# Optimization experiments

Hardware: AMD Instinct MI355X
Metric: run time of the kernel (lower is better)

## Reference

```python
import jax, jax.numpy as jnp
import numpy as np

B, S, E, H = 4, 2048, 1024, 16
D = E // H  # head_size = 64

def setup_inputs() -> dict:
    key = jax.random.key(0)
    ks = jax.random.split(key, 10)
    s_e = E ** -0.5
    s_4e = (4 * E) ** -0.5
    inp = {
        "x": jax.random.normal(ks[0], (B, S, E), dtype=jnp.float32),
        # per-head Q/K/V weights, stacked: [H, E, D], no bias
        "Wq": jax.random.normal(ks[1], (H, E, D), dtype=jnp.float32) * s_e,
        "Wk": jax.random.normal(ks[2], (H, E, D), dtype=jnp.float32) * s_e,
        "Wv": jax.random.normal(ks[3], (H, E, D), dtype=jnp.float32) * s_e,
        "Wo": jax.random.normal(ks[4], (E, E), dtype=jnp.float32) * s_e,
        "bo": jax.random.normal(ks[5], (E,), dtype=jnp.float32) * 0.01,
        "W1": jax.random.normal(ks[6], (E, 4 * E), dtype=jnp.float32) * s_e,
        "b1": jax.random.normal(ks[7], (4 * E,), dtype=jnp.float32) * 0.01,
        "W2": jax.random.normal(ks[8], (4 * E, E), dtype=jnp.float32) * s_4e,
        "b2": jax.random.normal(ks[9], (E,), dtype=jnp.float32) * 0.01,
    }
    return inp

def reference(x, Wq, Wk, Wv, Wo, bo, W1, b1, W2, b2):
    b, s, e = x.shape
    # NOTE: original scales by embedding_size**-0.5 (Size of x), not head_size
    scale = e ** -0.5
    q = jnp.einsum("bse,hed->bhsd", x, Wq)
    k = jnp.einsum("bse,hed->bhsd", x, Wk)
    v = jnp.einsum("bse,hed->bhsd", x, Wv)
    scores = jnp.einsum("bhsd,bhtd->bhst", q, k) * scale
    causal = jnp.tril(jnp.ones((s, s), dtype=bool))
    scores = jnp.where(causal, scores, -jnp.inf)
    weights = jax.nn.softmax(scores, axis=-1)
    attn = jnp.einsum("bhst,bhtd->bhsd", weights, v)  # [B,H,S,D]
    # concat heads along last dim: [B,S,H*D]
    attn = attn.transpose(0, 2, 1, 3).reshape(b, s, e)
    y = attn @ Wo + bo
    x = x + y  # residual (no LayerNorm applied in original forward)
    h = jax.nn.relu(x @ W1 + b1)
    ffn = h @ W2 + b2
    return x + ffn
```

## Files before the change

### kernel.cpp

```cpp
#include <hip/hip_runtime.h>
#include <stdint.h>

#define B_ 4
#define S_ 2048
#define E_ 1024
#define H_ 16
#define D_ 64

typedef unsigned short u16;
typedef u16 u16x8 __attribute__((ext_vector_type(8)));
typedef __bf16 bf16x8 __attribute__((ext_vector_type(8)));
typedef float f32x4 __attribute__((ext_vector_type(4)));

__device__ __forceinline__ float bf2f(u16 x) {
  unsigned int v = ((unsigned int)x) << 16;
  return __builtin_bit_cast(float, v);
}
__device__ __forceinline__ u16 f2bf(float f) {
  unsigned int u = __builtin_bit_cast(unsigned int, f);
  unsigned int r = (u + 0x7fffu + ((u >> 16) & 1u)) >> 16;
  return (u16)r;
}

__device__ __forceinline__ void gl2lds16(const u16* g, u16* l) {
  __builtin_amdgcn_global_load_lds(
      (const __attribute__((address_space(1))) void*)g,
      (__attribute__((address_space(3))) void*)l, 16, 0, 0);
}

__global__ __launch_bounds__(256) void cast_bf16_k(const float* __restrict__ src,
                                                   u16* __restrict__ dst, long n) {
  long i = ((long)blockIdx.x * 256 + threadIdx.x) * 8;
  if (i + 8 <= n) {
    f32x4 a = *(const f32x4*)(src + i), b = *(const f32x4*)(src + i + 4);
    u16x8 o;
#pragma unroll
    for (int j = 0; j < 4; j++) { o[j] = f2bf(a[j]); o[j + 4] = f2bf(b[j]); }
    *(u16x8*)(dst + i) = o;
  }
}

__global__ __launch_bounds__(256) void castT_k(const float* __restrict__ src,
                                               u16* __restrict__ dst, int R, int C) {
  long bofs = (long)blockIdx.z * R * C;
  src += bofs; dst += bofs;
  __shared__ u16 t[32][33];
  int c0 = blockIdx.x * 32, r0 = blockIdx.y * 32;
  int lc = threadIdx.x & 31, lr8 = threadIdx.x >> 5;
#pragma unroll
  for (int i = 0; i < 4; i++) {
    int lr = lr8 + i * 8;
    t[lr][lc] = f2bf(src[(long)(r0 + lr) * C + c0 + lc]);
  }
  __syncthreads();
#pragma unroll
  for (int i = 0; i < 4; i++) {
    int lr = lr8 + i * 8;
    dst[(long)(c0 + lr) * R + r0 + lc] = t[lc][lr];
  }
}

__global__ __launch_bounds__(256) void vT_k(const u16* __restrict__ QKV,
                                            u16* __restrict__ VTg) {
  int bh = blockIdx.z, d0 = blockIdx.y * 32, t0 = blockIdx.x * 32;
  int b = bh >> 4, h = bh & 15;
  __shared__ u16 t[32][33];
  int lc = threadIdx.x & 31, lr8 = threadIdx.x >> 5;
#pragma unroll
  for (int i = 0; i < 4; i++) {
    int lr = lr8 + i * 8;
    t[lr][lc] = QKV[(long)(b * S_ + t0 + lr) * 3072 + 2048 + h * 64 + d0 + lc];
  }
  __syncthreads();
#pragma unroll
  for (int i = 0; i < 4; i++) {
    int lr = lr8 + i * 8;
    VTg[((long)bh * 64 + d0 + lr) * S_ + t0 + lc] = t[lc][lr];
  }
}

template <bool AF32, bool CF32>
__global__ __launch_bounds__(256) void gemm128(const void* __restrict__ Av,
                                               const u16* __restrict__ BT,
                                               void* __restrict__ Cv,
                                               const float* __restrict__ bias,
                                               const float* __restrict__ resid,
                                               int M, int N, int K, int relu,
                                               u16* __restrict__ Cbf) {
  __shared__ u16 As[128 * 32];
  __shared__ u16 Bs[128 * 32];
  const int tid = threadIdx.x;
  const int wave = tid >> 6, lane = tid & 63;
  const int m0 = blockIdx.y * 128, n0 = blockIdx.x * 128;
  const int wm = wave >> 1, wn = wave & 1;
  const int fr = lane & 15, quad = lane >> 4;

  f32x4 acc[4][4] = {};

  const int srow = wave * 32 + (lane >> 2);
  const int skcol = (lane & 3) * 8;

  for (int k0 = 0; k0 < K; k0 += 32) {
    __syncthreads();
    if (AF32) {
      const float* Ap = (const float*)Av + (long)(m0 + (tid >> 1)) * K + k0 + (tid & 1) * 16;
      f32x4 f0 = *(const f32x4*)Ap, f1 = *(const f32x4*)(Ap + 4);
      f32x4 f2 = *(const f32x4*)(Ap + 8), f3 = *(const f32x4*)(Ap + 12);
      u16x8 p0, p1;
#pragma unroll
      for (int j = 0; j < 4; j++) {
        p0[j] = f2bf(f0[j]); p0[j + 4] = f2bf(f1[j]);
        p1[j] = f2bf(f2[j]); p1[j + 4] = f2bf(f3[j]);
      }
      *(u16x8*)&As[(tid >> 1) * 32 + (tid & 1) * 16] = p0;
      *(u16x8*)&As[(tid >> 1) * 32 + (tid & 1) * 16 + 8] = p1;
    } else {
      const u16* Ag = (const u16*)Av + (long)(m0 + srow) * K + k0 + skcol;
      gl2lds16(Ag, &As[(wave * 32) * 32]);
      gl2lds16(Ag + 16 * (long)K, &As[(wave * 32 + 16) * 32]);
    }
    {
      const u16* Bg = BT + (long)(n0 + srow) * K + k0 + skcol;
      gl2lds16(Bg, &Bs[(wave * 32) * 32]);
      gl2lds16(Bg + 16 * (long)K, &Bs[(wave * 32 + 16) * 32]);
    }
    __syncthreads();

    bf16x8 af[4], bfr[4];
#pragma unroll
    for (int mi = 0; mi < 4; mi++)
      af[mi] = __builtin_bit_cast(bf16x8, *(const u16x8*)&As[(wm * 64 + mi * 16 + fr) * 32 + quad * 8]);
#pragma unroll
    for (int ni = 0; ni < 4; ni++)
      bfr[ni] = __builtin_bit_cast(bf16x8, *(const u16x8*)&Bs[(wn * 64 + ni * 16 + fr) * 32 + quad * 8]);
#pragma unroll
    for (int mi = 0; mi < 4; mi++)
#pragma unroll
      for (int ni = 0; ni < 4; ni++)
        acc[mi][ni] = __builtin_amdgcn_mfma_f32_16x16x32_bf16(af[mi], bfr[ni], acc[mi][ni], 0, 0, 0);
  }

#pragma unroll
  for (int mi = 0; mi < 4; mi++)
#pragma unroll
    for (int ni = 0; ni < 4; ni++)
#pragma unroll
      for (int r = 0; r < 4; r++) {
        int gm = m0 + wm * 64 + mi * 16 + quad * 4 + r;
        int gn = n0 + wn * 64 + ni * 16 + fr;
        float v = acc[mi][ni][r];
        if (bias) v += bias[gn];
        if (resid) v += resid[(long)gm * N + gn];
        if (relu) v = fmaxf(v, 0.f);
        if (CF32) ((float*)Cv)[(long)gm * N + gn] = v;
        else      ((u16*)Cv)[(long)gm * N + gn] = f2bf(v);
        if (Cbf) Cbf[(long)gm * N + gn] = f2bf(v);
      }
}

__global__ __launch_bounds__(256) void attn_mfma3(const u16* __restrict__ QKV,
                                                  const u16* __restrict__ VTg,
                                                  u16* __restrict__ attn) {
  int p = blockIdx.x, h = blockIdx.y, b = blockIdx.z;
  int tid = threadIdx.x;
  int wq = tid >> 6, lane = tid & 63;
  int fr = lane & 15, quad = lane >> 4;
  int kf = quad * 8;

  __shared__ u16 Qs[64][72];
  __shared__ u16 Ks[64][72];
  __shared__ u16 Vt[64][72];
  __shared__ u16 Ps[4][16][72];

  const u16* base = QKV + (long)b * S_ * 3072;
  const u16* vbase = VTg + (long)(b * 16 + h) * 64 * S_;
  int st = tid >> 2;
  int sd = (tid & 3) * 16;

  for (int ti = 0; ti < 2; ti++) {
    int qt = ti ? (31 - p) : p;

    {
      const u16* qr = base + (long)(qt * 64 + st) * 3072 + h * 64 + sd;
      u16x8 a = *(const u16x8*)qr, d = *(const u16x8*)(qr + 8);
      u16x8 oa, od;
#pragma unroll
      for (int j = 0; j < 8; j++) {
        oa[j] = f2bf(bf2f(a[j]) * 0.03125f);
        od[j] = f2bf(bf2f(d[j]) * 0.03125f);
      }
      *(u16x8*)&Qs[st][sd] = oa;
      *(u16x8*)&Qs[st][sd + 8] = od;
    }
    __syncthreads();
    bf16x8 qf0 = __builtin_bit_cast(bf16x8, *(const u16x8*)&Qs[wq * 16 + fr][kf]);
    bf16x8 qf1 = __builtin_bit_cast(bf16x8, *(const u16x8*)&Qs[wq * 16 + fr][32 + kf]);

    f32x4 acc[4] = {};
    float m[4], l[4];
#pragma unroll
    for (int r = 0; r < 4; r++) { m[r] = -INFINITY; l[r] = 0.f; }

    for (int c = 0; c <= qt; c++) {
      int t0 = c * 64;
      __syncthreads();
      {
        const u16* kr = base + (long)(t0 + st) * 3072 + 1024 + h * 64 + sd;
        u16x8 k0 = *(const u16x8*)kr, k1 = *(const u16x8*)(kr + 8);
        const u16* vr = vbase + (long)st * S_ + t0 + sd;
        u16x8 v0 = *(const u16x8*)vr, v1 = *(const u16x8*)(vr + 8);
        *(u16x8*)&Ks[st][sd] = k0;
        *(u16x8*)&Ks[st][sd + 8] = k1;
        *(u16x8*)&Vt[st][sd] = v0;
        *(u16x8*)&Vt[st][sd + 8] = v1;
      }
      __syncthreads();

      f32x4 sc[4] = {};
#pragma unroll
      for (int nt = 0; nt < 4; nt++) {
        bf16x8 b0 = __builtin_bit_cast(bf16x8, *(const u16x8*)&Ks[nt * 16 + fr][kf]);
        bf16x8 b1 = __builtin_bit_cast(bf16x8, *(const u16x8*)&Ks[nt * 16 + fr][32 + kf]);
        sc[nt] = __builtin_amdgcn_mfma_f32_16x16x32_bf16(qf0, b0, sc[nt], 0, 0, 0);
        sc[nt] = __builtin_amdgcn_mfma_f32_16x16x32_bf16(qf1, b1, sc[nt], 0, 0, 0);
      }

      if (c == qt) {
        int qloc = wq * 16 + quad * 4;
#pragma unroll
        for (int nt = 0; nt < 4; nt++)
#pragma unroll
          for (int r = 0; r < 4; r++)
            if (nt * 16 + fr > qloc + r) sc[nt][r] = -1e30f;
      }

      float al[4], ps[4];
#pragma unroll
      for (int r = 0; r < 4; r++) {
        float v = fmaxf(fmaxf(sc[0][r], sc[1][r]), fmaxf(sc[2][r], sc[3][r]));
#pragma unroll
        for (int off = 1; off < 16; off <<= 1) v = fmaxf(v, __shfl_xor(v, off));
        float mn = fmaxf(m[r], v);
        al[r] = __expf(m[r] - mn);
        m[r] = mn;
        ps[r] = 0.f;
      }
#pragma unroll
      for (int nt = 0; nt < 4; nt++)
#pragma unroll
        for (int r = 0; r < 4; r++) {
          float pv = __expf(sc[nt][r] - m[r]);
          sc[nt][r] = pv;
          ps[r] += pv;
        }
#pragma unroll
      for (int r = 0; r < 4; r++) {
#pragma unroll
        for (int off = 1; off < 16; off <<= 1) ps[r] += __shfl_xor(ps[r], off);
        l[r] = l[r] * al[r] + ps[r];
#pragma unroll
        for (int nt = 0; nt < 4; nt++) acc[nt][r] *= al[r];
      }

#pragma unroll
      for (int nt = 0; nt < 4; nt++)
#pragma unroll
        for (int r = 0; r < 4; r++)
          Ps[wq][quad * 4 + r][nt * 16 + fr] = f2bf(sc[nt][r]);

      bf16x8 pa0 = __builtin_bit_cast(bf16x8, *(const u16x8*)&Ps[wq][fr][kf]);
      bf16x8 pa1 = __builtin_bit_cast(bf16x8, *(const u16x8*)&Ps[wq][fr][32 + kf]);
#pragma unroll
      for (int nt = 0; nt < 4; nt++) {
        bf16x8 vb0 = __builtin_bit_cast(bf16x8, *(const u16x8*)&Vt[nt * 16 + fr][kf]);
        bf16x8 vb1 = __builtin_bit_cast(bf16x8, *(const u16x8*)&Vt[nt * 16 + fr][32 + kf]);
        acc[nt] = __builtin_amdgcn_mfma_f32_16x16x32_bf16(pa0, vb0, acc[nt], 0, 0, 0);
        acc[nt] = __builtin_amdgcn_mfma_f32_16x16x32_bf16(pa1, vb1, acc[nt], 0, 0, 0);
      }
    }

    long row = (long)b * S_ + qt * 64 + wq * 16 + quad * 4;
#pragma unroll
    for (int nt = 0; nt < 4; nt++)
#pragma unroll
      for (int r = 0; r < 4; r++)
        attn[(row + r) * 1024 + h * 64 + nt * 16 + fr] = f2bf(acc[nt][r] / l[r]);
  }
}

extern "C" void kernel_launch(void* const* d_in, const int* in_sizes, int n_in,
                              void* d_out, int out_size, void* d_ws, size_t ws_size,
                              hipStream_t stream) {
  (void)in_sizes; (void)n_in; (void)out_size;
  const float* x  = (const float*)d_in[0];
  const float* Wq = (const float*)d_in[1];
  const float* Wk = (const float*)d_in[2];
  const float* Wv = (const float*)d_in[3];
  const float* Wo = (const float*)d_in[4];
  const float* bo = (const float*)d_in[5];
  const float* W1 = (const float*)d_in[6];
  const float* b1 = (const float*)d_in[7];
  const float* W2 = (const float*)d_in[8];
  const float* b2 = (const float*)d_in[9];
  float* out = (float*)d_out;

  char* ws = (char*)d_ws;
  u16*   QKV  = (u16*)(ws);
  u16*   attn = (u16*)(ws + 50331648);
  u16*   hbuf = (u16*)(ws);
  float* x1   = (float*)(ws + 67108864);
  u16*   VTg  = (u16*)(ws + 67108864);
  u16*   xb   = (u16*)(ws + 83886080);
  u16*   WT   = (u16*)(ws + 100663296);
  u16*   WoT  = (u16*)(ws + 106954752);
  u16*   W1T  = (u16*)(ws + 109051904);
  u16*   W2T  = (u16*)(ws + 117440512);
  u16*   x1b  = (u16*)(ws + 125829120);
  bool bigws = ws_size >= (size_t)142606336;

  cast_bf16_k<<<4096, 256, 0, stream>>>(x, xb, (long)8192 * 1024);
  castT_k<<<dim3(2, 32, 16), 256, 0, stream>>>(Wq, WT, 1024, 64);
  castT_k<<<dim3(2, 32, 16), 256, 0, stream>>>(Wk, WT + 1048576, 1024, 64);
  castT_k<<<dim3(2, 32, 16), 256, 0, stream>>>(Wv, WT + 2097152, 1024, 64);
  castT_k<<<dim3(32, 32, 1), 256, 0, stream>>>(Wo, WoT, 1024, 1024);
  castT_k<<<dim3(128, 32, 1), 256, 0, stream>>>(W1, W1T, 1024, 4096);
  castT_k<<<dim3(32, 128, 1), 256, 0, stream>>>(W2, W2T, 4096, 1024);

  gemm128<false, false><<<dim3(24, 64), 256, 0, stream>>>(xb, WT, QKV, nullptr, nullptr, 8192, 3072, 1024, 0, nullptr);
  vT_k<<<dim3(64, 2, 64), 256, 0, stream>>>(QKV, VTg);
  attn_mfma3<<<dim3(16, H_, B_), 256, 0, stream>>>(QKV, VTg, attn);
  gemm128<false, true><<<dim3(8, 64), 256, 0, stream>>>(attn, WoT, x1, bo, x, 8192, 1024, 1024, 0, bigws ? x1b : nullptr);
  if (bigws)
    gemm128<false, false><<<dim3(32, 64), 256, 0, stream>>>(x1b, W1T, hbuf, b1, nullptr, 8192, 4096, 1024, 1, nullptr);
  else
    gemm128<true, false><<<dim3(32, 64), 256, 0, stream>>>(x1, W1T, hbuf, b1, nullptr, 8192, 4096, 1024, 1, nullptr);
  gemm128<false, true><<<dim3(8, 64), 256, 0, stream>>>(hbuf, W2T, out, b2, x1, 8192, 1024, 4096, 0, nullptr);
}
```

Baseline: 667.5 us.

## Add 256x256 tiled bf16 MFMA GEMM with XCD swizzle and staged double buffering

Introduces a 512-thread GEMM kernel with 256x256 output tiles, 128 KB of LDS double-buffered in 64-wide K steps, a swizzled LDS layout, and global-to-LDS staging interleaved with four MFMA phases per K step using setprio and explicit waitcnt. Workgroup IDs are remapped so consecutive tiles land on the same XCD. It replaces the 128x128 GEMM for the QKV, output-projection, FFN1 and FFN2 launches. The aim is more operand reuse per LDS load and overlap of memory traffic with compute. The cost is heavy register pressure and fewer workgroups per GEMM (128 for the N=1024 GEMMs), which may underfill the GPU.

```diff
diff --git a/kernel.cpp b/kernel.cpp
--- a/kernel.cpp
+++ b/kernel.cpp
@@ -158,6 +158,177 @@
       }
 }
 
+__device__ __forceinline__ bf16x8 ldfrag(const u16* base, int r, int kk, int quad) {
+  int u = (((r << 5) + (quad << 3) + (kk << 13)) ^ (((r >> 3) & 1) << 4));
+  return __builtin_bit_cast(bf16x8, *(const u16x8*)(base + u));
+}
+
+__device__ __forceinline__ void stage_half_g(const u16* __restrict__ G, int ldk,
+                                             int row0, int k0,
+                                             u16* __restrict__ region,
+                                             int half, int tid) {
+  int r = half * 128 + (tid >> 2);
+  int c = ((tid & 3) << 3) ^ (((r >> 3) & 1) << 4);
+  const u16* g = G + (size_t)(row0 + r) * ldk + k0 + c;
+  u16* l = region + half * 4096 + (tid >> 6) * 512;
+  gl2lds16(g, l);
+  gl2lds16(g + 32, l + 8192);
+}
+
+template <bool CF32>
+__global__ __launch_bounds__(512) void gemm256(const u16* __restrict__ A,
+                                               const u16* __restrict__ BT,
+                                               void* __restrict__ Cv,
+                                               const float* __restrict__ bias,
+                                               const float* __restrict__ resid,
+                                               int M, int N, int K, int relu,
+                                               u16* __restrict__ Cbf) {
+  (void)M;
+  __shared__ u16 sm[65536];
+  const int tid = threadIdx.x;
+  const int wave = tid >> 6, lane = tid & 63;
+  const int wm = wave >> 2, wn = wave & 3;
+  const int fr = lane & 15, quad = lane >> 4;
+
+  const int nbx = gridDim.x;
+  const int nwg = nbx * (int)gridDim.y;
+  const int wgid = blockIdx.y * nbx + blockIdx.x;
+  const int qq = nwg >> 3, rr = nwg & 7;
+  const int xcd = wgid & 7, loc = wgid >> 3;
+  const int sw = (xcd < rr ? xcd * (qq + 1) : rr * (qq + 1) + (xcd - rr) * qq) + loc;
+  const int n0 = (sw % nbx) * 256;
+  const int m0 = (sw / nbx) * 256;
+
+  const int NT = K >> 6;
+
+  f32x4 acc[8][4] = {};
+
+  u16* buf0 = sm;
+  u16* buf1 = sm + 32768;
+
+  stage_half_g(A, K, m0, 0, buf0, 0, tid);
+  stage_half_g(A, K, m0, 0, buf0, 1, tid);
+  stage_half_g(BT, K, n0, 0, buf0 + 16384, 0, tid);
+  stage_half_g(BT, K, n0, 0, buf0 + 16384, 1, tid);
+  if (NT > 1) {
+    stage_half_g(A, K, m0, 64, buf1, 0, tid);
+    stage_half_g(A, K, m0, 64, buf1, 1, tid);
+    asm volatile("s_waitcnt vmcnt(4)" ::: "memory");
+  } else {
+    asm volatile("s_waitcnt vmcnt(0)" ::: "memory");
+  }
+  __builtin_amdgcn_s_barrier();
+
+  for (int t = 0; t < NT; ++t) {
+    u16* cb = (t & 1) ? buf1 : buf0;
+    u16* nb = (t & 1) ? buf0 : buf1;
+    const int kn = (t + 1) << 6;
+    const int k2 = (t + 2) << 6;
+    const bool st1 = (t + 1) < NT;
+    const bool st2 = (t + 2) < NT;
+
+    bf16x8 a0[4][2], a1[4][2], b0[2][2], b1[2][2];
+
+#pragma unroll
+    for (int mi = 0; mi < 4; ++mi)
+#pragma unroll
+      for (int kk = 0; kk < 2; ++kk)
+        a0[mi][kk] = ldfrag(cb, wm * 128 + mi * 16 + fr, kk, quad);
+#pragma unroll
+    for (int ni = 0; ni < 2; ++ni)
+#pragma unroll
+      for (int kk = 0; kk < 2; ++kk)
+        b0[ni][kk] = ldfrag(cb + 16384, wn * 64 + ni * 16 + fr, kk, quad);
+    if (st1) stage_half_g(BT, K, n0, kn, nb + 16384, 0, tid);
+    __builtin_amdgcn_s_barrier();
+    asm volatile("s_waitcnt lgkmcnt(0)" ::: "memory");
+    __builtin_amdgcn_sched_barrier(0);
+    __builtin_amdgcn_s_setprio(1);
+#pragma unroll
+    for (int mi = 0; mi < 4; ++mi)
+#pragma unroll
+      for (int ni = 0; ni < 2; ++ni)
+#pragma unroll
+        for (int kk = 0; kk < 2; ++kk)
+          acc[mi][ni] = __builtin_amdgcn_mfma_f32_16x16x32_bf16(a0[mi][kk], b0[ni][kk], acc[mi][ni], 0, 0, 0);
+    __builtin_amdgcn_s_setprio(0);
+    __builtin_amdgcn_s_barrier();
+
+#pragma unroll
+    for (int mi = 0; mi < 4; ++mi)
+#pragma unroll
+      for (int kk = 0; kk < 2; ++kk)
+        a1[mi][kk] = ldfrag(cb, wm * 128 + (mi + 4) * 16 + fr, kk, quad);
+    if (st1) stage_half_g(BT, K, n0, kn, nb + 16384, 1, tid);
+    __builtin_amdgcn_s_barrier();
+    asm volatile("s_waitcnt lgkmcnt(0)" ::: "memory");
+    __builtin_amdgcn_sched_barrier(0);
+    __builtin_amdgcn_s_setprio(1);
+#pragma unroll
+    for (int mi = 0; mi < 4; ++mi)
+#pragma unroll
+      for (int ni = 0; ni < 2; ++ni)
+#pragma unroll
+        for (int kk = 0; kk < 2; ++kk)
+          acc[mi + 4][ni] = __builtin_amdgcn_mfma_f32_16x16x32_bf16(a1[mi][kk], b0[ni][kk], acc[mi + 4][ni], 0, 0, 0);
+    __builtin_amdgcn_s_setprio(0);
+    __builtin_amdgcn_s_barrier();
+
+#pragma unroll
+    for (int ni = 0; ni < 2; ++ni)
+#pragma unroll
+      for (int kk = 0; kk < 2; ++kk)
+        b1[ni][kk] = ldfrag(cb + 16384, wn * 64 + (ni + 2) * 16 + fr, kk, quad);
+    if (st2) stage_half_g(A, K, m0, k2, cb, 0, tid);
+    __builtin_amdgcn_s_barrier();
+    asm volatile("s_waitcnt lgkmcnt(0)" ::: "memory");
+    __builtin_amdgcn_sched_barrier(0);
+    __builtin_amdgcn_s_setprio(1);
+#pragma unroll
+    for (int mi = 0; mi < 4; ++mi)
+#pragma unroll
+      for (int ni = 0; ni < 2; ++ni)
+#pragma unroll
+        for (int kk = 0; kk < 2; ++kk)
+          acc[mi + 4][ni + 2] = __builtin_amdgcn_mfma_f32_16x16x32_bf16(a1[mi][kk], b1[ni][kk], acc[mi + 4][ni + 2], 0, 0, 0);
+    __builtin_amdgcn_s_setprio(0);
+    __builtin_amdgcn_s_barrier();
+
+    if (st2) stage_half_g(A, K, m0, k2, cb, 1, tid);
+    if (st2) asm volatile("s_waitcnt vmcnt(4)" ::: "memory");
+    else     asm volatile("s_waitcnt vmcnt(0)" ::: "memory");
+    __builtin_amdgcn_s_barrier();
+    __builtin_amdgcn_sched_barrier(0);
+    __builtin_amdgcn_s_setprio(1);
+#pragma unroll
+    for (int mi = 0; mi < 4; ++mi)
+#pragma unroll
+      for (int ni = 0; ni < 2; ++ni)
+#pragma unroll
+        for (int kk = 0; kk < 2; ++kk)
+          acc[mi][ni + 2] = __builtin_amdgcn_mfma_f32_16x16x32_bf16(a0[mi][kk], b1[ni][kk], acc[mi][ni + 2], 0, 0, 0);
+    __builtin_amdgcn_s_setprio(0);
+    __builtin_amdgcn_s_barrier();
+  }
+
+#pragma unroll
+  for (int mi = 0; mi < 8; ++mi)
+#pragma unroll
+    for (int ni = 0; ni < 4; ++ni)
+#pragma unroll
+      for (int r = 0; r < 4; ++r) {
+        int gm = m0 + wm * 128 + mi * 16 + quad * 4 + r;
+        int gn = n0 + wn * 64 + ni * 16 + fr;
+        float v = acc[mi][ni][r];
+        if (bias) v += bias[gn];
+        if (resid) v += resid[(long)gm * N + gn];
+        if (relu) v = fmaxf(v, 0.f);
+        if (CF32) ((float*)Cv)[(long)gm * N + gn] = v;
+        else      ((u16*)Cv)[(long)gm * N + gn] = f2bf(v);
+        if (Cbf) Cbf[(long)gm * N + gn] = f2bf(v);
+      }
+}
+
 __global__ __launch_bounds__(256) void attn_mfma3(const u16* __restrict__ QKV,
                                                   const u16* __restrict__ VTg,
                                                   u16* __restrict__ attn) {
@@ -326,13 +497,13 @@
   castT_k<<<dim3(128, 32, 1), 256, 0, stream>>>(W1, W1T, 1024, 4096);
   castT_k<<<dim3(32, 128, 1), 256, 0, stream>>>(W2, W2T, 4096, 1024);
 
-  gemm128<false, false><<<dim3(24, 64), 256, 0, stream>>>(xb, WT, QKV, nullptr, nullptr, 8192, 3072, 1024, 0, nullptr);
+  gemm256<false><<<dim3(12, 32), 512, 0, stream>>>(xb, WT, QKV, nullptr, nullptr, 8192, 3072, 1024, 0, nullptr);
   vT_k<<<dim3(64, 2, 64), 256, 0, stream>>>(QKV, VTg);
   attn_mfma3<<<dim3(16, H_, B_), 256, 0, stream>>>(QKV, VTg, attn);
-  gemm128<false, true><<<dim3(8, 64), 256, 0, stream>>>(attn, WoT, x1, bo, x, 8192, 1024, 1024, 0, bigws ? x1b : nullptr);
+  gemm256<true><<<dim3(4, 32), 512, 0, stream>>>(attn, WoT, x1, bo, x, 8192, 1024, 1024, 0, bigws ? x1b : nullptr);
   if (bigws)
-    gemm128<false, false><<<dim3(32, 64), 256, 0, stream>>>(x1b, W1T, hbuf, b1, nullptr, 8192, 4096, 1024, 1, nullptr);
+    gemm256<false><<<dim3(16, 32), 512, 0, stream>>>(x1b, W1T, hbuf, b1, nullptr, 8192, 4096, 1024, 1, nullptr);
   else
     gemm128<true, false><<<dim3(32, 64), 256, 0, stream>>>(x1, W1T, hbuf, b1, nullptr, 8192, 4096, 1024, 1, nullptr);
-  gemm128<false, true><<<dim3(8, 64), 256, 0, stream>>>(hbuf, W2T, out, b2, x1, 8192, 1024, 4096, 0, nullptr);
-}
+  gemm256<true><<<dim3(4, 32), 512, 0, stream>>>(hbuf, W2T, out, b2, x1, 8192, 1024, 4096, 0, nullptr);
+}
```

After: 702.1 us. 5.2% more time.

## Replace 128-tile GEMMs with 256-row 512-thread pipelined GEMM kernel

Applied to the files above, without the earlier changes.

Adds a new gemm256 kernel with 256xBN tiles, 8 waves, and double-buffered direct global-to-LDS staging using XOR swizzle. It interleaves MFMA quadrants with next-tile loads, raises wave priority around MFMAs, and remaps workgroups for XCD locality. The QKV, output projection, FFN1 and FFN2 GEMMs switch to it. The larger tiles raise data reuse, but they use more LDS and registers and leave fewer workgroups for the smaller GEMMs.

```diff
diff --git a/kernel.cpp b/kernel.cpp
--- a/kernel.cpp
+++ b/kernel.cpp
@@ -158,6 +158,163 @@
       }
 }
 
+__device__ __forceinline__ bf16x8 ldfragS(const u16* base, int r, int kk, int quad, int SL) {
+  int u = (((r << 5) + (quad << 3) + kk * SL)) ^ (((r >> 3) & 1) << 4);
+  return __builtin_bit_cast(bf16x8, *(const u16x8*)(base + u));
+}
+
+__device__ __forceinline__ void stage_half(const u16* __restrict__ G, int ldk,
+                                           int row0, int k0,
+                                           u16* __restrict__ region,
+                                           int half, int tid, int SLu) {
+  int r = half * 128 + (tid >> 2);
+  int c = ((tid & 3) << 3) ^ (((r >> 3) & 1) << 4);
+  const u16* g = G + (size_t)(row0 + r) * ldk + k0 + c;
+  u16* l = region + half * 4096 + (tid >> 6) * 512;
+  gl2lds16(g, l);
+  gl2lds16(g + 32, l + SLu);
+}
+
+#define MFMA_Q(ML, NL)                                                         \
+  __builtin_amdgcn_s_setprio(1);                                               \
+  _Pragma("unroll") for (int mi = 0; mi < MH; ++mi)                            \
+  _Pragma("unroll") for (int ni = 0; ni < NH; ++ni)                            \
+  _Pragma("unroll") for (int kk = 0; kk < 2; ++kk)                             \
+      acc[(ML) + mi][(NL) + ni] = __builtin_amdgcn_mfma_f32_16x16x32_bf16(     \
+          aF[(ML) + mi][kk], bF[(NL) + ni][kk], acc[(ML) + mi][(NL) + ni],     \
+          0, 0, 0);                                                            \
+  __builtin_amdgcn_s_setprio(0);
+
+template <int BN, bool CF32>
+__global__ __launch_bounds__(512) void gemm256(const u16* __restrict__ A,
+                                               const u16* __restrict__ BT,
+                                               void* __restrict__ Cv,
+                                               const float* __restrict__ bias,
+                                               const float* __restrict__ resid,
+                                               int M, int N, int K, int relu,
+                                               u16* __restrict__ Cbf) {
+  (void)M;
+  constexpr int WM = (BN == 256) ? 2 : 4;
+  constexpr int WN = 8 / WM;
+  constexpr int MI = 256 / (WM * 16);
+  constexpr int NI = BN / (WN * 16);
+  constexpr int MH = MI / 2, NH = NI / 2;
+  constexpr int BSL = BN * 32;
+  constexpr int BUFU = 16384 + BN * 64;
+  constexpr int BH = BN / 128;
+  constexpr int NREADS = (MI + NI) * 2;
+
+  __shared__ u16 sm[2 * BUFU];
+  const int tid = threadIdx.x;
+  const int wave = tid >> 6, lane = tid & 63;
+  const int wm = wave / WN, wn = wave % WN;
+  const int fr = lane & 15, quad = lane >> 4;
+
+  const int nbx = gridDim.x;
+  const int nwg = nbx * (int)gridDim.y;
+  const int wgid = blockIdx.y * nbx + blockIdx.x;
+  const int qq = nwg >> 3, rr = nwg & 7;
+  const int xcd = wgid & 7, loc = wgid >> 3;
+  const int sw = (xcd < rr ? xcd * (qq + 1) : rr * (qq + 1) + (xcd - rr) * qq) + loc;
+  const int n0 = (sw % nbx) * BN;
+  const int m0 = (sw / nbx) * 256;
+
+  const int NT = K >> 6;
+
+  f32x4 acc[MI][NI] = {};
+
+  u16* buf0 = sm;
+  u16* buf1 = sm + BUFU;
+
+  const int rAbase = wm * (256 / WM) + fr;
+  const int rBbase = wn * 64 + fr;
+
+  stage_half(A, K, m0, 0, buf0, 0, tid, 8192);
+  stage_half(A, K, m0, 0, buf0, 1, tid, 8192);
+  stage_half(BT, K, n0, 0, buf0 + 16384, 0, tid, BSL);
+  if (BH == 2) stage_half(BT, K, n0, 0, buf0 + 16384, 1, tid, BSL);
+  if (NT > 1) {
+    stage_half(A, K, m0, 64, buf1, 0, tid, 8192);
+    stage_half(A, K, m0, 64, buf1, 1, tid, 8192);
+    stage_half(BT, K, n0, 64, buf1 + 16384, 0, tid, BSL);
+    if (BH == 2) stage_half(BT, K, n0, 64, buf1 + 16384, 1, tid, BSL);
+    if constexpr (BN == 256) asm volatile("s_waitcnt vmcnt(8)" ::: "memory");
+    else                     asm volatile("s_waitcnt vmcnt(6)" ::: "memory");
+  } else {
+    asm volatile("s_waitcnt vmcnt(0)" ::: "memory");
+  }
+  __builtin_amdgcn_s_barrier();
+
+  for (int t = 0; t < NT; ++t) {
+    u16* cb = (t & 1) ? buf1 : buf0;
+    const int k2 = (t + 2) << 6;
+    const bool st2 = (t + 2) < NT;
+
+    bf16x8 aF[MI][2], bF[NI][2];
+
+#pragma unroll
+    for (int mi = 0; mi < MH; ++mi)
+#pragma unroll
+      for (int kk = 0; kk < 2; ++kk)
+        aF[mi][kk] = ldfragS(cb, rAbase + mi * 16, kk, quad, 8192);
+#pragma unroll
+    for (int ni = 0; ni < NH; ++ni)
+#pragma unroll
+      for (int kk = 0; kk < 2; ++kk)
+        bF[ni][kk] = ldfragS(cb + 16384, rBbase + ni * 16, kk, quad, BSL);
+#pragma unroll
+    for (int mi = MH; mi < MI; ++mi)
+#pragma unroll
+      for (int kk = 0; kk < 2; ++kk)
+        aF[mi][kk] = ldfragS(cb, rAbase + mi * 16, kk, quad, 8192);
+#pragma unroll
+    for (int ni = NH; ni < NI; ++ni)
+#pragma unroll
+      for (int kk = 0; kk < 2; ++kk)
+        bF[ni][kk] = ldfragS(cb + 16384, rBbase + ni * 16, kk, quad, BSL);
+    __builtin_amdgcn_sched_group_barrier(0x100 , NREADS, 0);
+
+    MFMA_Q(0, 0)
+    MFMA_Q(MH, 0)
+    __builtin_amdgcn_s_barrier();
+    if (st2) {
+      stage_half(A, K, m0, k2, cb, 0, tid, 8192);
+      stage_half(A, K, m0, k2, cb, 1, tid, 8192);
+    }
+    MFMA_Q(MH, NH)
+    __builtin_amdgcn_s_barrier();
+    if (st2) {
+      stage_half(BT, K, n0, k2, cb + 16384, 0, tid, BSL);
+      if (BH == 2) stage_half(BT, K, n0, k2, cb + 16384, 1, tid, BSL);
+    }
+    MFMA_Q(0, NH)
+    if (st2) {
+      if constexpr (BN == 256) asm volatile("s_waitcnt vmcnt(8)" ::: "memory");
+      else                     asm volatile("s_waitcnt vmcnt(6)" ::: "memory");
+    } else {
+      asm volatile("s_waitcnt vmcnt(0)" ::: "memory");
+    }
+    __builtin_amdgcn_s_barrier();
+  }
+
+#pragma unroll
+  for (int mi = 0; mi < MI; ++mi)
+#pragma unroll
+    for (int ni = 0; ni < NI; ++ni)
+#pragma unroll
+      for (int r = 0; r < 4; ++r) {
+        int gm = m0 + wm * (256 / WM) + mi * 16 + quad * 4 + r;
+        int gn = n0 + wn * 64 + ni * 16 + fr;
+        float v = acc[mi][ni][r];
+        if (bias) v += bias[gn];
+        if (resid) v += resid[(long)gm * N + gn];
+        if (relu) v = fmaxf(v, 0.f);
+        if (CF32) ((float*)Cv)[(long)gm * N + gn] = v;
+        else      ((u16*)Cv)[(long)gm * N + gn] = f2bf(v);
+        if (Cbf) Cbf[(long)gm * N + gn] = f2bf(v);
+      }
+}
+
 __global__ __launch_bounds__(256) void attn_mfma3(const u16* __restrict__ QKV,
                                                   const u16* __restrict__ VTg,
                                                   u16* __restrict__ attn) {
@@ -326,13 +483,13 @@
   castT_k<<<dim3(128, 32, 1), 256, 0, stream>>>(W1, W1T, 1024, 4096);
   castT_k<<<dim3(32, 128, 1), 256, 0, stream>>>(W2, W2T, 4096, 1024);
 
-  gemm128<false, false><<<dim3(24, 64), 256, 0, stream>>>(xb, WT, QKV, nullptr, nullptr, 8192, 3072, 1024, 0, nullptr);
+  gemm256<128, false><<<dim3(24, 32), 512, 0, stream>>>(xb, WT, QKV, nullptr, nullptr, 8192, 3072, 1024, 0, nullptr);
   vT_k<<<dim3(64, 2, 64), 256, 0, stream>>>(QKV, VTg);
   attn_mfma3<<<dim3(16, H_, B_), 256, 0, stream>>>(QKV, VTg, attn);
-  gemm128<false, true><<<dim3(8, 64), 256, 0, stream>>>(attn, WoT, x1, bo, x, 8192, 1024, 1024, 0, bigws ? x1b : nullptr);
+  gemm256<128, true><<<dim3(8, 32), 512, 0, stream>>>(attn, WoT, x1, bo, x, 8192, 1024, 1024, 0, bigws ? x1b : nullptr);
   if (bigws)
-    gemm128<false, false><<<dim3(32, 64), 256, 0, stream>>>(x1b, W1T, hbuf, b1, nullptr, 8192, 4096, 1024, 1, nullptr);
+    gemm256<256, false><<<dim3(16, 32), 512, 0, stream>>>(x1b, W1T, hbuf, b1, nullptr, 8192, 4096, 1024, 1, nullptr);
   else
     gemm128<true, false><<<dim3(32, 64), 256, 0, stream>>>(x1, W1T, hbuf, b1, nullptr, 8192, 4096, 1024, 1, nullptr);
-  gemm128<false, true><<<dim3(8, 64), 256, 0, stream>>>(hbuf, W2T, out, b2, x1, 8192, 1024, 4096, 0, nullptr);
-}
+  gemm256<128, true><<<dim3(8, 32), 512, 0, stream>>>(hbuf, W2T, out, b2, x1, 8192, 1024, 4096, 0, nullptr);
+}
```

Result: faster. 587.9 us (-11.9%).
